# Optimization experiments

Measured on AMD Instinct MI355X. Metric: run time of the kernel, lower is better.

## Reference

```python
import jax, jax.numpy as jnp
import numpy as np

# Dims: batch=2, seqlen=L=384, d_inner=d=384, d_state=s=384, dt_rank=r=384, d_conv=4.
# NOTE: the original torch module only runs when L == d_inner == d_state == dt_rank
# (see its broadcasting in SelectiveScan and the Linear layer plumbing); we reproduce
# that exact (quirky) broadcast faithfully.
B_, L_, D_, S_, R_, K_ = 2, 384, 384, 384, 384, 4


def setup_inputs() -> dict:
    key = jax.random.key(0)
    ks = jax.random.split(key, 9)
    f32 = jnp.float32
    return {
        "x": jax.random.normal(ks[0], (B_, L_, D_), f32),
        "A_log": jax.random.normal(ks[1], (D_, S_), f32) * 0.02,
        "D": jax.random.normal(ks[2], (D_,), f32) * 0.02,
        "dt_w": jax.random.normal(ks[3], (D_, R_), f32) * 0.02,
        "dt_b": jax.random.normal(ks[4], (D_,), f32) * 0.02,
        "B_w": jax.random.normal(ks[5], (S_, D_), f32) * (1.0 / np.sqrt(D_)),
        "C_w": jax.random.normal(ks[6], (S_, D_), f32) * (1.0 / np.sqrt(D_)),
        "conv_w": jax.random.normal(ks[7], (D_, 1, K_), f32) * (1.0 / np.sqrt(K_)),
        "conv_b": jnp.zeros((D_,), f32),
    }


def _forward(x, A_log, D, dt_w, dt_b, B_w, C_w, conv_w, conv_b):
    b, L, d = x.shape
    A = -jnp.exp(A_log)                       # (d, s)
    dt = jax.nn.softplus(x @ dt_w.T + dt_b)   # (b, L, d)
    x_dbl = x @ B_w.T                         # (b, L, s)
    Bm = x_dbl @ B_w.T                        # (b, L, s)  (module applies B_proj twice)
    Cm = x_dbl @ C_w.T                        # (b, L, s)
    # causal depthwise conv1d: pad (k-1) on the left == torch pad k-1 then [:, :, :L]
    xc = jax.lax.conv_general_dilated(
        x.transpose(0, 2, 1), conv_w, (1,), [(conv_w.shape[-1] - 1, 0)],
        feature_group_count=d, dimension_numbers=("NCH", "OIH", "NCH"))
    xc = xc + conv_b[None, :, None]
    u = jax.nn.silu(xc.transpose(0, 2, 1))    # (b, L, d)
    # selective scan (faithful to the torch SelectiveScan broadcasting)
    deltaA = jnp.exp(dt[..., None] * A[None, None])          # (b, L, d, s)
    deltaB_u = dt[..., None] * Bm[:, None, :, :] * u[..., None]  # (b, L, d, s), needs L==d

    def step(h, inp):
        dA_i, dBu_i, C_i, u_i = inp
        h = dA_i * h + dBu_i                  # (b, d, s)
        y = jnp.sum(h * C_i[:, None, :], -1) + u_i * D  # (b, d)
        return h, y

    h0 = jnp.zeros((b, d, deltaA.shape[-1]), x.dtype)
    xs = (deltaA.transpose(1, 0, 2, 3), deltaB_u.transpose(1, 0, 2, 3),
          Cm.transpose(1, 0, 2), u.transpose(1, 0, 2))
    _, ys = jax.lax.scan(step, h0, xs)        # ys: (L, b, d)
    return ys.transpose(1, 0, 2)


def reference(x, A_log, D, dt_w, dt_b, B_w, C_w, conv_w, conv_b):
    return _forward(x, A_log, D, dt_w, dt_b, B_w, C_w, conv_w, conv_b)
```

## Files before the change

### kernel.cpp

```cpp
#include <hip/hip_runtime.h>
#include <math.h>

#define B_SZ 2
#define L_SZ 384
#define D_SZ 384
#define S_SZ 384
#define BLK_ELEMS (L_SZ * D_SZ)
#define TOT_ELEMS (B_SZ * L_SZ * D_SZ)
#define LOG2E 1.4426950408889634f

typedef __attribute__((ext_vector_type(8))) short bf16x8;
typedef __attribute__((ext_vector_type(4))) float f32x4;

__device__ __forceinline__ float fexp2(float x) {
  return __builtin_amdgcn_exp2f(x);
}
__device__ __forceinline__ float softplus_f(float z) {
  return (z > 20.f) ? z : log1pf(__expf(z));
}
__device__ __forceinline__ unsigned short f2bf(float f) {
  unsigned int u = __float_as_uint(f);
  return (unsigned short)((u + 0x7FFFu + ((u >> 16) & 1u)) >> 16);
}
#define PIPELINE_FENCE() asm volatile("" ::: "memory")

__global__ __launch_bounds__(256) void cvt_bf16_kernel(
    const float* __restrict__ x, const float* __restrict__ dt_w,
    const float* __restrict__ B_w, const float* __restrict__ C_w,
    unsigned short* __restrict__ xbf, unsigned short* __restrict__ dtwbf,
    unsigned short* __restrict__ Bwbf, unsigned short* __restrict__ Cwbf) {
  const int blk = blockIdx.x;
  const float* src;
  unsigned short* dst;
  int base;
  if (blk < 288) { src = x; dst = xbf; base = blk; }
  else if (blk < 432) { src = dt_w; dst = dtwbf; base = blk - 288; }
  else if (blk < 576) { src = B_w; dst = Bwbf; base = blk - 432; }
  else { src = C_w; dst = Cwbf; base = blk - 576; }
  const int idx = base * 1024 + threadIdx.x * 4;
  const float4 v = *(const float4*)(src + idx);
  ushort4 o;
  o.x = f2bf(v.x); o.y = f2bf(v.y); o.z = f2bf(v.z); o.w = f2bf(v.w);
  *(ushort4*)(dst + idx) = o;
}

template <int MODE>
__global__ __launch_bounds__(256) void mfma_dual_gemm(
    const unsigned short* __restrict__ Abf,
    const unsigned short* __restrict__ W1bf,
    const unsigned short* __restrict__ W2bf,
    const float* __restrict__ bias,
    float* __restrict__ O1, void* __restrict__ O2v) {
  const int wid = ((blockIdx.x << 8) + (int)threadIdx.x) >> 6;
  const int mt = wid / 24;
  const int nt = wid - mt * 24;
  const int lane = threadIdx.x & 63;
  const int rc = lane & 15;
  const int quad = lane >> 4;

  const unsigned short* ap = Abf + (mt * 16 + rc) * 384 + quad * 8;
  const unsigned short* w1p = W1bf + (nt * 16 + rc) * 384 + quad * 8;
  const unsigned short* w2p = W2bf + (nt * 16 + rc) * 384 + quad * 8;

  bf16x8 af[12], w1f[12], w2f[12];
#pragma unroll
  for (int kt = 0; kt < 12; ++kt) {
    af[kt] = *(const bf16x8*)(ap + kt * 32);
    w1f[kt] = *(const bf16x8*)(w1p + kt * 32);
    w2f[kt] = *(const bf16x8*)(w2p + kt * 32);
  }
  PIPELINE_FENCE();
  f32x4 acc1 = {0.f, 0.f, 0.f, 0.f};
  f32x4 acc2 = {0.f, 0.f, 0.f, 0.f};
#pragma unroll
  for (int kt = 0; kt < 12; ++kt) {
    acc1 = __builtin_amdgcn_mfma_f32_16x16x32_bf16(af[kt], w1f[kt], acc1, 0, 0, 0);
    acc2 = __builtin_amdgcn_mfma_f32_16x16x32_bf16(af[kt], w2f[kt], acc2, 0, 0, 0);
  }
  const int col = nt * 16 + rc;
  const int row0 = mt * 16 + quad * 4;
  if constexpr (MODE == 1) {
    unsigned short* O2 = (unsigned short*)O2v;
    const float bb = bias[col];
#pragma unroll
    for (int r = 0; r < 4; ++r) {
      O1[(row0 + r) * 384 + col] = softplus_f(acc1[r] + bb);
      O2[(row0 + r) * 384 + col] = f2bf(acc2[r]);
    }
  } else {
    float* O2 = (float*)O2v;
#pragma unroll
    for (int r = 0; r < 4; ++r) {
      O1[(row0 + r) * 384 + col] = acc1[r];
      O2[(row0 + r) * 384 + col] = acc2[r];
    }
  }
}

__global__ __launch_bounds__(256) void conv_silu_kernel(
    const float* __restrict__ x, const float* __restrict__ cw,
    const float* __restrict__ cb, const float* __restrict__ dt,
    float* __restrict__ u, float* __restrict__ dtu) {
  const int idx = blockIdx.x * 256 + threadIdx.x;
  const int i = idx % D_SZ;
  const int l = (idx / D_SZ) % L_SZ;
  const int b = idx / BLK_ELEMS;
  float acc = cb[i];
#pragma unroll
  for (int t = 0; t < 4; t++) {
    const int ls = l - 3 + t;
    const float xv = (ls >= 0) ? x[(b * L_SZ + ls) * D_SZ + i] : 0.f;
    acc = fmaf(xv, cw[i * 4 + t], acc);
  }
  const float uv = acc / (1.f + __expf(-acc));
  u[idx] = uv;
  dtu[idx] = dt[idx] * uv;
}

#define CH 8
__global__ __launch_bounds__(64, 3) void scan_kernel(
    const float* __restrict__ A_log, const float* __restrict__ dt,
    const float* __restrict__ dtu, const float* __restrict__ Bm,
    const float* __restrict__ Cm, float* __restrict__ p0,
    float* __restrict__ p1, float* __restrict__ p2) {
  const int bid = blockIdx.x;
  const int sid = bid / 3;
  const int w = bid % 3;
  const int b = sid / D_SZ;
  const int i = sid % D_SZ;
  const int lane = threadIdx.x;
  const int j0 = w * 128 + 2 * lane;

  const float2 av = *(const float2*)(A_log + i * S_SZ + j0);
  const float2 bv = *(const float2*)(Bm + (b * D_SZ + i) * S_SZ + j0);
  const float a20 = -__expf(av.x) * LOG2E;
  const float a21 = -__expf(av.y) * LOG2E;
  const float bw0 = bv.x, bw1 = bv.y;
  float h0 = 0.f, h1 = 0.f;

  const float* dtp = dt + b * BLK_ELEMS + i;
  const float* dup = dtu + b * BLK_ELEMS + i;
  const float* cp = Cm + b * BLK_ELEMS + j0;
  float* psel = (w == 0) ? p0 : ((w == 1) ? p1 : p2);
  float* pp = psel + (b * D_SZ + i) * L_SZ;

  const int sidx = ((lane & 1) << 2) | (lane & 2) | ((lane >> 2) & 1);
  const bool storer = lane < 8;

  float C0[16], D0[8], U0[8];
  float C1[16], D1[8], U1[8];
  float C2[16], D2[8], U2[8];

  auto load_chunk = [&](int c, float (&cx)[16], float (&dx)[8],
                        float (&ux)[8]) {
    const int l0 = c * CH;
#pragma unroll
    for (int s = 0; s < CH; ++s) {
      const int l = (l0 + s < L_SZ) ? (l0 + s) : (L_SZ - 1);
      dx[s] = dtp[l * D_SZ];
      ux[s] = dup[l * D_SZ];
      const float2 c2 = *(const float2*)(cp + l * D_SZ);
      cx[2 * s] = c2.x;
      cx[2 * s + 1] = c2.y;
    }
  };

  auto compute_chunk = [&](int c, const float (&cx)[16], const float (&dx)[8],
                           const float (&ux)[8]) {
    float accs[8];
#pragma unroll
    for (int s = 0; s < CH; ++s) {
      const float dts = dx[s];
      const float dtus = ux[s];
      const float e0 = fexp2(dts * a20);
      const float e1 = fexp2(dts * a21);
      h0 = fmaf(e0, h0, bw0 * dtus);
      h1 = fmaf(e1, h1, bw1 * dtus);
      accs[s] = fmaf(h1, cx[2 * s + 1], h0 * cx[2 * s]);
    }
    {
      const bool s1 = (lane & 1) != 0;
#pragma unroll
      for (int q = 0; q < 4; ++q) {
        const float keep = s1 ? accs[q + 4] : accs[q];
        const float send = s1 ? accs[q] : accs[q + 4];
        accs[q] = keep + __shfl_xor(send, 1, 64);
      }
      const bool s2 = (lane & 2) != 0;
#pragma unroll
      for (int q = 0; q < 2; ++q) {
        const float keep = s2 ? accs[q + 2] : accs[q];
        const float send = s2 ? accs[q] : accs[q + 2];
        accs[q] = keep + __shfl_xor(send, 2, 64);
      }
      const bool s3 = (lane & 4) != 0;
      {
        const float keep = s3 ? accs[1] : accs[0];
        const float send = s3 ? accs[0] : accs[1];
        accs[0] = keep + __shfl_xor(send, 4, 64);
      }
    }
    float r = accs[0];
    r += __shfl_xor(r, 8, 64);
    r += __shfl_xor(r, 16, 64);
    r += __shfl_xor(r, 32, 64);
    if (storer) pp[c * CH + sidx] = r;
  };

  load_chunk(0, C0, D0, U0);
  load_chunk(1, C1, D1, U1);
  for (int it = 0; it < 16; ++it) {
    const int c = 3 * it;
    load_chunk((c + 2 < 48) ? c + 2 : 47, C2, D2, U2);
    PIPELINE_FENCE();
    compute_chunk(c, C0, D0, U0);
    load_chunk((c + 3 < 48) ? c + 3 : 47, C0, D0, U0);
    PIPELINE_FENCE();
    compute_chunk(c + 1, C1, D1, U1);
    load_chunk((c + 4 < 48) ? c + 4 : 47, C1, D1, U1);
    PIPELINE_FENCE();
    compute_chunk(c + 2, C2, D2, U2);
  }
}

__global__ __launch_bounds__(256) void combine_kernel(
    const float* __restrict__ p0, const float* __restrict__ p1,
    const float* __restrict__ p2, const float* __restrict__ u,
    const float* __restrict__ Dv, float* __restrict__ y) {
  __shared__ float T[32][33];
  const int tx = threadIdx.x;
  const int ty0 = threadIdx.y;
  const int b = blockIdx.z;
  const int i0 = blockIdx.y * 32;
  const int l0 = blockIdx.x * 32;
#pragma unroll
  for (int r = 0; r < 4; ++r) {
    const int il = ty0 + 8 * r;
    const int off = (b * D_SZ + i0 + il) * L_SZ + l0 + tx;
    T[il][tx] = p0[off] + p1[off] + p2[off];
  }
  __syncthreads();
#pragma unroll
  for (int r = 0; r < 4; ++r) {
    const int ll = ty0 + 8 * r;
    const int gi = i0 + tx;
    const int off = (b * L_SZ + l0 + ll) * D_SZ + gi;
    y[off] = fmaf(u[off], Dv[gi], T[tx][ll]);
  }
}

extern "C" void kernel_launch(void* const* d_in, const int* in_sizes, int n_in,
                              void* d_out, int out_size, void* d_ws,
                              size_t ws_size, hipStream_t stream) {
  const float* x = (const float*)d_in[0];
  const float* A_log = (const float*)d_in[1];
  const float* D = (const float*)d_in[2];
  const float* dt_w = (const float*)d_in[3];
  const float* dt_b = (const float*)d_in[4];
  const float* B_w = (const float*)d_in[5];
  const float* C_w = (const float*)d_in[6];
  const float* conv_w = (const float*)d_in[7];
  const float* conv_b = (const float*)d_in[8];
  float* y = (float*)d_out;

  float* ws = (float*)d_ws;
  float* dt = ws;
  float* p0 = ws + TOT_ELEMS;
  float* Bm = ws + 2 * TOT_ELEMS;
  float* Cm = ws + 3 * TOT_ELEMS;
  float* u = ws + 4 * TOT_ELEMS;
  float* dtu = ws + 5 * TOT_ELEMS;
  float* p1 = ws + 6 * TOT_ELEMS;
  float* p2 = ws + 7 * TOT_ELEMS;
  unsigned short* bfarea = (unsigned short*)(ws + 8 * TOT_ELEMS);
  unsigned short* xbf = bfarea;
  unsigned short* dtwbf = bfarea + 294912;
  unsigned short* Bwbf = bfarea + 442368;
  unsigned short* Cwbf = bfarea + 589824;
  unsigned short* xdblbf = bfarea + 737280;

  cvt_bf16_kernel<<<720, 256, 0, stream>>>(x, dt_w, B_w, C_w, xbf, dtwbf, Bwbf, Cwbf);
  mfma_dual_gemm<1><<<288, 256, 0, stream>>>(xbf, dtwbf, Bwbf, dt_b, dt, xdblbf);
  mfma_dual_gemm<2><<<288, 256, 0, stream>>>(xdblbf, Bwbf, Cwbf, nullptr, Bm, Cm);
  conv_silu_kernel<<<TOT_ELEMS / 256, 256, 0, stream>>>(x, conv_w, conv_b, dt, u, dtu);
  scan_kernel<<<3 * B_SZ * D_SZ, 64, 0, stream>>>(A_log, dt, dtu, Bm, Cm, p0, p1, p2);
  combine_kernel<<<dim3(L_SZ / 32, D_SZ / 32, B_SZ), dim3(32, 8), 0, stream>>>(
      p0, p1, p2, u, D, y);
}
```

Baseline: 155.6 us.

## Split scan state across six waves per channel and transpose dt inputs

The scan now gives each (batch, channel) six 64-lane wavefronts, one state element per lane, where before it used three waves with two states per lane. This doubles the wave count and halves the serial work per lane to expose more parallelism. The conv kernel now also writes dt and dt*u transposed to [b,d,L] through shared memory, so the scan can read them with contiguous float4 loads instead of strided scalar loads. The costs are six partial-sum buffers that the combine kernel must read and add, a larger workspace, and an occupancy hint added to the GEMM.

```diff
diff --git a/kernel.cpp b/kernel.cpp
--- a/kernel.cpp
+++ b/kernel.cpp
@@ -45,7 +45,7 @@
 }
 
 template <int MODE>
-__global__ __launch_bounds__(256) void mfma_dual_gemm(
+__global__ __launch_bounds__(256, 2) void mfma_dual_gemm(
     const unsigned short* __restrict__ Abf,
     const unsigned short* __restrict__ W1bf,
     const unsigned short* __restrict__ W2bf,
@@ -97,86 +97,98 @@
   }
 }
 
-__global__ __launch_bounds__(256) void conv_silu_kernel(
+__global__ __launch_bounds__(256) void conv_tr_kernel(
     const float* __restrict__ x, const float* __restrict__ cw,
     const float* __restrict__ cb, const float* __restrict__ dt,
-    float* __restrict__ u, float* __restrict__ dtu) {
-  const int idx = blockIdx.x * 256 + threadIdx.x;
-  const int i = idx % D_SZ;
-  const int l = (idx / D_SZ) % L_SZ;
-  const int b = idx / BLK_ELEMS;
-  float acc = cb[i];
-#pragma unroll
-  for (int t = 0; t < 4; t++) {
-    const int ls = l - 3 + t;
-    const float xv = (ls >= 0) ? x[(b * L_SZ + ls) * D_SZ + i] : 0.f;
-    acc = fmaf(xv, cw[i * 4 + t], acc);
-  }
-  const float uv = acc / (1.f + __expf(-acc));
-  u[idx] = uv;
-  dtu[idx] = dt[idx] * uv;
+    float* __restrict__ u, float* __restrict__ dt_t,
+    float* __restrict__ dtu_t) {
+  __shared__ float Tdt[32][33];
+  __shared__ float Tdu[32][33];
+  const int tx = threadIdx.x;
+  const int ty = threadIdx.y;
+  const int b = blockIdx.z;
+  const int i0 = blockIdx.y * 32;
+  const int l0 = blockIdx.x * 32;
+  const int gi = i0 + tx;
+  const float cbv = cb[gi];
+  const float cw0 = cw[gi * 4 + 0], cw1 = cw[gi * 4 + 1];
+  const float cw2 = cw[gi * 4 + 2], cw3 = cw[gi * 4 + 3];
+#pragma unroll
+  for (int r = 0; r < 4; ++r) {
+    const int l = l0 + ty + 8 * r;
+    float acc = cbv;
+    const float x3 = x[(b * L_SZ + l) * D_SZ + gi];
+    const float x2 = (l >= 1) ? x[(b * L_SZ + l - 1) * D_SZ + gi] : 0.f;
+    const float x1 = (l >= 2) ? x[(b * L_SZ + l - 2) * D_SZ + gi] : 0.f;
+    const float x0 = (l >= 3) ? x[(b * L_SZ + l - 3) * D_SZ + gi] : 0.f;
+    acc = fmaf(x0, cw0, acc);
+    acc = fmaf(x1, cw1, acc);
+    acc = fmaf(x2, cw2, acc);
+    acc = fmaf(x3, cw3, acc);
+    const float uv = acc / (1.f + __expf(-acc));
+    const int off = (b * L_SZ + l) * D_SZ + gi;
+    u[off] = uv;
+    const float dtv = dt[off];
+    Tdt[ty + 8 * r][tx] = dtv;
+    Tdu[ty + 8 * r][tx] = dtv * uv;
+  }
+  __syncthreads();
+#pragma unroll
+  for (int r = 0; r < 4; ++r) {
+    const int il = ty + 8 * r;
+    const int off = (b * D_SZ + i0 + il) * L_SZ + l0 + tx;
+    dt_t[off] = Tdt[tx][il];
+    dtu_t[off] = Tdu[tx][il];
+  }
 }
 
 #define CH 8
-__global__ __launch_bounds__(64, 3) void scan_kernel(
-    const float* __restrict__ A_log, const float* __restrict__ dt,
-    const float* __restrict__ dtu, const float* __restrict__ Bm,
-    const float* __restrict__ Cm, float* __restrict__ p0,
-    float* __restrict__ p1, float* __restrict__ p2) {
-  const int bid = blockIdx.x;
-  const int sid = bid / 3;
-  const int w = bid % 3;
+__global__ __launch_bounds__(256, 4) void scan_kernel(
+    const float* __restrict__ A_log, const float* __restrict__ dt_t,
+    const float* __restrict__ dtu_t, const float* __restrict__ Bm,
+    const float* __restrict__ Cm, float* __restrict__ part) {
+  const int wid = ((blockIdx.x << 8) + (int)threadIdx.x) >> 6;
+  const int lane = threadIdx.x & 63;
+  const int w = wid % 6;
+  const int sid = wid / 6;
   const int b = sid / D_SZ;
   const int i = sid % D_SZ;
-  const int lane = threadIdx.x;
-  const int j0 = w * 128 + 2 * lane;
-
-  const float2 av = *(const float2*)(A_log + i * S_SZ + j0);
-  const float2 bv = *(const float2*)(Bm + (b * D_SZ + i) * S_SZ + j0);
-  const float a20 = -__expf(av.x) * LOG2E;
-  const float a21 = -__expf(av.y) * LOG2E;
-  const float bw0 = bv.x, bw1 = bv.y;
-  float h0 = 0.f, h1 = 0.f;
-
-  const float* dtp = dt + b * BLK_ELEMS + i;
-  const float* dup = dtu + b * BLK_ELEMS + i;
-  const float* cp = Cm + b * BLK_ELEMS + j0;
-  float* psel = (w == 0) ? p0 : ((w == 1) ? p1 : p2);
-  float* pp = psel + (b * D_SZ + i) * L_SZ;
+  const int j = w * 64 + lane;
+
+  const float a2 = -__expf(A_log[i * S_SZ + j]) * LOG2E;
+  const float bw = Bm[(b * D_SZ + i) * S_SZ + j];
+  float h = 0.f;
+
+  const float* dtp = dt_t + (b * D_SZ + i) * L_SZ;
+  const float* dup = dtu_t + (b * D_SZ + i) * L_SZ;
+  const float* cp = Cm + b * BLK_ELEMS + j;
+  float* pp = part + ((w * B_SZ + b) * D_SZ + i) * L_SZ;
 
   const int sidx = ((lane & 1) << 2) | (lane & 2) | ((lane >> 2) & 1);
   const bool storer = lane < 8;
 
-  float C0[16], D0[8], U0[8];
-  float C1[16], D1[8], U1[8];
-  float C2[16], D2[8], U2[8];
-
-  auto load_chunk = [&](int c, float (&cx)[16], float (&dx)[8],
-                        float (&ux)[8]) {
+  float C0[8], D0[8], U0[8];
+  float C1[8], D1[8], U1[8];
+  float C2[8], D2[8], U2[8];
+
+  auto load_chunk = [&](int c, float (&cx)[8], float (&dx)[8], float (&ux)[8]) {
     const int l0 = c * CH;
-#pragma unroll
-    for (int s = 0; s < CH; ++s) {
-      const int l = (l0 + s < L_SZ) ? (l0 + s) : (L_SZ - 1);
-      dx[s] = dtp[l * D_SZ];
-      ux[s] = dup[l * D_SZ];
-      const float2 c2 = *(const float2*)(cp + l * D_SZ);
-      cx[2 * s] = c2.x;
-      cx[2 * s + 1] = c2.y;
-    }
+    *(float4*)&dx[0] = *(const float4*)(dtp + l0);
+    *(float4*)&dx[4] = *(const float4*)(dtp + l0 + 4);
+    *(float4*)&ux[0] = *(const float4*)(dup + l0);
+    *(float4*)&ux[4] = *(const float4*)(dup + l0 + 4);
+#pragma unroll
+    for (int s = 0; s < CH; ++s) cx[s] = cp[(l0 + s) * D_SZ];
   };
 
-  auto compute_chunk = [&](int c, const float (&cx)[16], const float (&dx)[8],
+  auto compute_chunk = [&](int c, const float (&cx)[8], const float (&dx)[8],
                            const float (&ux)[8]) {
     float accs[8];
 #pragma unroll
     for (int s = 0; s < CH; ++s) {
-      const float dts = dx[s];
-      const float dtus = ux[s];
-      const float e0 = fexp2(dts * a20);
-      const float e1 = fexp2(dts * a21);
-      h0 = fmaf(e0, h0, bw0 * dtus);
-      h1 = fmaf(e1, h1, bw1 * dtus);
-      accs[s] = fmaf(h1, cx[2 * s + 1], h0 * cx[2 * s]);
+      const float e = fexp2(dx[s] * a2);
+      h = fmaf(e, h, bw * ux[s]);
+      accs[s] = h * cx[s];
     }
     {
       const bool s1 = (lane & 1) != 0;
@@ -224,8 +236,7 @@
 }
 
 __global__ __launch_bounds__(256) void combine_kernel(
-    const float* __restrict__ p0, const float* __restrict__ p1,
-    const float* __restrict__ p2, const float* __restrict__ u,
+    const float* __restrict__ part, const float* __restrict__ u,
     const float* __restrict__ Dv, float* __restrict__ y) {
   __shared__ float T[32][33];
   const int tx = threadIdx.x;
@@ -236,8 +247,11 @@
 #pragma unroll
   for (int r = 0; r < 4; ++r) {
     const int il = ty0 + 8 * r;
-    const int off = (b * D_SZ + i0 + il) * L_SZ + l0 + tx;
-    T[il][tx] = p0[off] + p1[off] + p2[off];
+    float s = 0.f;
+#pragma unroll
+    for (int w = 0; w < 6; ++w)
+      s += part[((w * B_SZ + b) * D_SZ + i0 + il) * L_SZ + l0 + tx];
+    T[il][tx] = s;
   }
   __syncthreads();
 #pragma unroll
@@ -265,14 +279,13 @@
 
   float* ws = (float*)d_ws;
   float* dt = ws;
-  float* p0 = ws + TOT_ELEMS;
+  float* u = ws + TOT_ELEMS;
   float* Bm = ws + 2 * TOT_ELEMS;
   float* Cm = ws + 3 * TOT_ELEMS;
-  float* u = ws + 4 * TOT_ELEMS;
-  float* dtu = ws + 5 * TOT_ELEMS;
-  float* p1 = ws + 6 * TOT_ELEMS;
-  float* p2 = ws + 7 * TOT_ELEMS;
-  unsigned short* bfarea = (unsigned short*)(ws + 8 * TOT_ELEMS);
+  float* dt_t = ws + 4 * TOT_ELEMS;
+  float* dtu_t = ws + 5 * TOT_ELEMS;
+  float* part = ws + 6 * TOT_ELEMS;
+  unsigned short* bfarea = (unsigned short*)(ws + 12 * TOT_ELEMS);
   unsigned short* xbf = bfarea;
   unsigned short* dtwbf = bfarea + 294912;
   unsigned short* Bwbf = bfarea + 442368;
@@ -282,8 +295,9 @@
   cvt_bf16_kernel<<<720, 256, 0, stream>>>(x, dt_w, B_w, C_w, xbf, dtwbf, Bwbf, Cwbf);
   mfma_dual_gemm<1><<<288, 256, 0, stream>>>(xbf, dtwbf, Bwbf, dt_b, dt, xdblbf);
   mfma_dual_gemm<2><<<288, 256, 0, stream>>>(xdblbf, Bwbf, Cwbf, nullptr, Bm, Cm);
-  conv_silu_kernel<<<TOT_ELEMS / 256, 256, 0, stream>>>(x, conv_w, conv_b, dt, u, dtu);
-  scan_kernel<<<3 * B_SZ * D_SZ, 64, 0, stream>>>(A_log, dt, dtu, Bm, Cm, p0, p1, p2);
+  conv_tr_kernel<<<dim3(L_SZ / 32, D_SZ / 32, B_SZ), dim3(32, 8), 0, stream>>>(
+      x, conv_w, conv_b, dt, u, dt_t, dtu_t);
+  scan_kernel<<<(6 * B_SZ * D_SZ) / 4, 256, 0, stream>>>(A_log, dt_t, dtu_t, Bm, Cm, part);
   combine_kernel<<<dim3(L_SZ / 32, D_SZ / 32, B_SZ), dim3(32, 8), 0, stream>>>(
-      p0, p1, p2, u, D, y);
-}
+      part, u, D, y);
+}
```

Result: slower. 160.5 us (+3.1%).
